# Optimization experiments

Measured on AMD Instinct MI355X. Metric: run time of the kernel, lower is better.

The kernel has to match this reference:

```python
import jax, jax.numpy as jnp
import numpy as np


def setup_inputs() -> dict:
    key = jax.random.key(0)
    kx, ky = jax.random.split(key)
    n, m, d = 2048, 2048, 16  # d == n_wires
    x = jax.random.normal(kx, (n, d), dtype=jnp.float32)
    y = jax.random.normal(ky, (m, d), dtype=jnp.float32)
    return {"x": x, "y": y}


def reference(x, y):
    # RY gates on distinct wires commute; RY(-y_k) RY(x_k) = RY(x_k - y_k).
    # State = tensor product over wires of RY(x_k - y_k)|0>, so the |0...0>
    # amplitude is prod_k cos((x_k - y_k)/2). Original code stores abs(amplitude).
    half_diff = 0.5 * (x[:, None, :] - y[None, :, :])  # [n, m, d]
    kernel = jnp.abs(jnp.prod(jnp.cos(half_diff), axis=-1))  # [n, m]
    return kernel
```

## Files before the change

### kernel.cpp

```cpp
#include <hip/hip_runtime.h>
#include <hip/hip_bf16.h>


constexpr int D = 16;
constexpr int RSTR = 72;

typedef short  bf16x8 __attribute__((ext_vector_type(8)));
typedef float  f32x4  __attribute__((ext_vector_type(4)));

static __device__ inline unsigned int pk2(float a, float b) {
    __hip_bfloat16 ha = __float2bfloat16(a);
    __hip_bfloat16 hb = __float2bfloat16(b);
    unsigned short ua, ub;
    __builtin_memcpy(&ua, &ha, 2);
    __builtin_memcpy(&ub, &hb, 2);
    return (unsigned int)ua | ((unsigned int)ub << 16);
}

__global__ __launch_bounds__(256)
void qkern(const float* __restrict__ x, const float* __restrict__ y,
           float* __restrict__ out, int m) {
    __shared__ unsigned short Al[64 * RSTR];
    __shared__ unsigned short Bl[64 * RSTR];

    const int tid  = threadIdx.x;
    const int row0b = blockIdx.x * 64;
    const int col0b = blockIdx.y * 64;

    {
        const int u    = tid >> 1;
        const int half = tid & 1;
        const bool isrow = (u < 64);
        const float* src = isrow ? (x + (size_t)(row0b + u) * D)
                                 : (y + (size_t)(col0b + (u - 64)) * D);
        unsigned short* dst = (isrow ? Al + (size_t)u * RSTR
                                     : Bl + (size_t)(u - 64) * RSTR);
        const float scale = isrow ? 0.5f : 1.0f;

        float f[4][4];
#pragma unroll
        for (int pp = 0; pp < 4; ++pp) {
            const int p = half * 4 + pp;
            const float a0 = src[2 * p], a1 = src[2 * p + 1];
            float sm, cm, sp, cp;
            __sincosf(0.5f * (a0 - a1), &sm, &cm);
            __sincosf(0.5f * (a0 + a1), &sp, &cp);
            f[pp][0] = scale * cm; f[pp][1] = scale * sm;
            f[pp][2] = scale * cp; f[pp][3] = scale * sp;
        }
#pragma unroll
        for (int qq = 0; qq < 2; ++qq) {
            const int q = half * 2 + qq;
            const float* fa = f[2 * qq];
            const float* fb = f[2 * qq + 1];
            uint4 lo, hi;
            lo.x = pk2(fa[0] * fb[0], fa[0] * fb[1]);
            lo.y = pk2(fa[0] * fb[2], fa[0] * fb[3]);
            lo.z = pk2(fa[1] * fb[0], fa[1] * fb[1]);
            lo.w = pk2(fa[1] * fb[2], fa[1] * fb[3]);
            hi.x = pk2(fa[2] * fb[0], fa[2] * fb[1]);
            hi.y = pk2(fa[2] * fb[2], fa[2] * fb[3]);
            hi.z = pk2(fa[3] * fb[0], fa[3] * fb[1]);
            hi.w = pk2(fa[3] * fb[2], fa[3] * fb[3]);
            *(uint4*)(dst + q * 16)     = lo;
            *(uint4*)(dst + q * 16 + 8) = hi;
        }
    }
    __syncthreads();

    const int wave = tid >> 6;
    const int lane = tid & 63;
    const int m16  = lane & 15;
    const int kh   = lane >> 4;
    const int rw0  = wave * 16;

    const bf16x8 zf = {0, 0, 0, 0, 0, 0, 0, 0};
    const f32x4  zc = {0.f, 0.f, 0.f, 0.f};

    bf16x8 af[4];
#pragma unroll
    for (int q = 0; q < 4; ++q)
        af[q] = (kh < 2)
            ? *(const bf16x8*)(Al + (size_t)(rw0 + m16) * RSTR + q * 16 + kh * 8)
            : zf;

#pragma unroll
    for (int cg = 0; cg < 4; ++cg) {
        f32x4 acc[4];
#pragma unroll
        for (int q = 0; q < 4; ++q) {
            const bf16x8 bfq = (kh < 2)
                ? *(const bf16x8*)(Bl + (size_t)(cg * 16 + m16) * RSTR + q * 16 + kh * 8)
                : zf;
            acc[q] = __builtin_amdgcn_mfma_f32_16x16x32_bf16(af[q], bfq, zc, 0, 0, 0);
        }
#pragma unroll
        for (int r = 0; r < 4; ++r) {
            const float v = fabsf(acc[0][r] * acc[1][r] * acc[2][r] * acc[3][r]);
            const int row = row0b + rw0 + kh * 4 + r;
            __builtin_nontemporal_store(v, out + (size_t)row * m + col0b + cg * 16 + m16);
        }
    }
}

extern "C" void kernel_launch(void* const* d_in, const int* in_sizes, int n_in,
                              void* d_out, int out_size, void* d_ws, size_t ws_size,
                              hipStream_t stream) {
    const float* x = (const float*)d_in[0];
    const float* y = (const float*)d_in[1];
    float* out = (float*)d_out;
    const int n = in_sizes[0] / D;
    const int m = in_sizes[1] / D;

    dim3 grid(n / 64, m / 64);
    qkern<<<grid, 256, 0, stream>>>(x, y, out, m);
}
```

Before: 62.22 us.

## Use 32x32x16 MFMA with swapped operands for vectorized row-wise stores

Replaces the 16x16x32 MFMA path, which zero-padded half of each K-slice, with 32x32x16 bf16 MFMAs that use the full 16-wide K per pair group. Each wave now covers a 32x32 tile. The A and B operands are swapped so each lane holds consecutive columns of one output row, which allows 128-bit nontemporal vector stores instead of scalar stores. This cuts wasted MFMA work and the number of store instructions, at the cost of larger per-lane accumulators.

```diff
diff --git a/kernel.cpp b/kernel.cpp
--- a/kernel.cpp
+++ b/kernel.cpp
@@ -6,7 +6,8 @@
 constexpr int RSTR = 72;
 
 typedef short  bf16x8 __attribute__((ext_vector_type(8)));
-typedef float  f32x4  __attribute__((ext_vector_type(4)));
+typedef float  f32x16 __attribute__((ext_vector_type(16)));
+typedef float  vf4    __attribute__((ext_vector_type(4)));
 
 static __device__ inline unsigned int pk2(float a, float b) {
     __hip_bfloat16 ha = __float2bfloat16(a);
@@ -23,7 +24,7 @@
     __shared__ unsigned short Al[64 * RSTR];
     __shared__ unsigned short Bl[64 * RSTR];
 
-    const int tid  = threadIdx.x;
+    const int tid   = threadIdx.x;
     const int row0b = blockIdx.x * 64;
     const int col0b = blockIdx.y * 64;
 
@@ -70,36 +71,37 @@
 
     const int wave = tid >> 6;
     const int lane = tid & 63;
-    const int m16  = lane & 15;
-    const int kh   = lane >> 4;
-    const int rw0  = wave * 16;
+    const int l31  = lane & 31;
+    const int kh   = lane >> 5;
+    const int rw   = (wave >> 1) * 32;
+    const int cw   = (wave & 1) * 32;
 
-    const bf16x8 zf = {0, 0, 0, 0, 0, 0, 0, 0};
-    const f32x4  zc = {0.f, 0.f, 0.f, 0.f};
+    const f32x16 zc = {0.f};
 
-    bf16x8 af[4];
+    f32x16 prod;
+    {
+        const bf16x8 a0 = *(const bf16x8*)(Bl + (size_t)(cw + l31) * RSTR + 0 * 16 + kh * 8);
+        const bf16x8 b0 = *(const bf16x8*)(Al + (size_t)(rw + l31) * RSTR + 0 * 16 + kh * 8);
+        prod = __builtin_amdgcn_mfma_f32_32x32x16_bf16(a0, b0, zc, 0, 0, 0);
+    }
 #pragma unroll
-    for (int q = 0; q < 4; ++q)
-        af[q] = (kh < 2)
-            ? *(const bf16x8*)(Al + (size_t)(rw0 + m16) * RSTR + q * 16 + kh * 8)
-            : zf;
+    for (int q = 1; q < 4; ++q) {
+        const bf16x8 aq = *(const bf16x8*)(Bl + (size_t)(cw + l31) * RSTR + q * 16 + kh * 8);
+        const bf16x8 bq = *(const bf16x8*)(Al + (size_t)(rw + l31) * RSTR + q * 16 + kh * 8);
+        const f32x16 acc = __builtin_amdgcn_mfma_f32_32x32x16_bf16(aq, bq, zc, 0, 0, 0);
+        prod *= acc;
+    }
 
+    const int orow = row0b + rw + l31;
+    float* rowp = out + (size_t)orow * m + col0b + cw + 4 * kh;
 #pragma unroll
-    for (int cg = 0; cg < 4; ++cg) {
-        f32x4 acc[4];
-#pragma unroll
-        for (int q = 0; q < 4; ++q) {
-            const bf16x8 bfq = (kh < 2)
-                ? *(const bf16x8*)(Bl + (size_t)(cg * 16 + m16) * RSTR + q * 16 + kh * 8)
-                : zf;
-            acc[q] = __builtin_amdgcn_mfma_f32_16x16x32_bf16(af[q], bfq, zc, 0, 0, 0);
-        }
-#pragma unroll
-        for (int r = 0; r < 4; ++r) {
-            const float v = fabsf(acc[0][r] * acc[1][r] * acc[2][r] * acc[3][r]);
-            const int row = row0b + rw0 + kh * 4 + r;
-            __builtin_nontemporal_store(v, out + (size_t)row * m + col0b + cg * 16 + m16);
-        }
+    for (int g = 0; g < 4; ++g) {
+        vf4 v;
+        v.x = fabsf(prod[4 * g + 0]);
+        v.y = fabsf(prod[4 * g + 1]);
+        v.z = fabsf(prod[4 * g + 2]);
+        v.w = fabsf(prod[4 * g + 3]);
+        __builtin_nontemporal_store(v, (vf4*)(rowp + 8 * g));
     }
 }
 
```

Result: slower. 69.33 us (+11.4%).
